# Optimization experiments

Measured on AMD Instinct MI355X. Metric: run time of the kernel, lower is better.

The kernel has to match this reference:

```python
import jax, jax.numpy as jnp
import numpy as np

B, L, KNN = 8, 512, 16
D, H, NL, DLAT = 1024, 16, 2, 64
DH = D // H
DFF = 4 * D
HENC = D // 2          # SwiGLUFFNEncoder hidden = d_model // 2
POS_CLIP = 32
NPOS = 2 * POS_CLIP + 1


def _layernorm(x, g, b, eps=1e-5):
    m = x.mean(-1, keepdims=True)
    v = ((x - m) ** 2).mean(-1, keepdims=True)
    return (x - m) / jnp.sqrt(v + eps) * g + b


def setup_inputs() -> dict:
    key = jax.random.key(0)
    ks = jax.random.split(key, 16)

    def g(i, shape, scale=0.02):
        return jax.random.normal(ks[i], shape, dtype=jnp.float32) * scale

    return {
        "coords": jax.random.normal(ks[0], (B, L, 3, 3), dtype=jnp.float32) * 3.0,
        "eps": jax.random.normal(ks[1], (B, L, DLAT), dtype=jnp.float32),
        "emb": g(2, (NPOS, D)),
        "ln1_g": jnp.ones((NL, D)), "ln1_b": jnp.zeros((NL, D)),
        "Wqkv": g(3, (NL, D, 3 * D)), "bqkv": jnp.zeros((NL, 3 * D)),
        "dist_scale": g(4, (NL, H), 1.0),
        "Wo": g(5, (NL, D, D)), "bo": jnp.zeros((NL, D)),
        "ln2_g": jnp.ones((NL, D)), "ln2_b": jnp.zeros((NL, D)),
        "Wf1": g(6, (NL, D, 2 * DFF)), "bf1": jnp.zeros((NL, 2 * DFF)),
        "Wf2": g(7, (NL, DFF, D)), "bf2": jnp.zeros((NL, D)),
        "lnf_g": jnp.ones((D,)), "lnf_b": jnp.zeros((D,)),
        "We1": g(8, (D, 2 * HENC)), "be1": jnp.zeros((2 * HENC,)),
        "We2": g(9, (HENC, 2 * DLAT)), "be2": jnp.zeros((2 * DLAT,)),
        "attention_mask": jnp.ones((B, L), dtype=bool),
        "sequence_id": jnp.zeros((B, L), dtype=jnp.int32),
    }


def reference(coords, eps, emb, ln1_g, ln1_b, Wqkv, bqkv, dist_scale, Wo, bo,
              ln2_g, ln2_b, Wf1, bf1, Wf2, bf2, lnf_g, lnf_b, We1, be1, We2, be2,
              attention_mask, sequence_id):
    # --- frames: only CA translations feed the geometric attention bias ---
    t = coords[..., 1, :]                       # CA atoms, [B,L,3]

    # --- KNN graph build (no_grad in torch -> stop_gradient) ---
    ca = jax.lax.stop_gradient(t)
    d2 = ((ca[:, :, None, :] - ca[:, None, :, :]) ** 2).sum(-1)   # [B,L,L]
    same_seq = sequence_id[:, :, None] == sequence_id[:, None, :]
    valid = attention_mask[:, None, :] & same_seq
    d2 = jnp.where(valid, d2, jnp.inf)
    _, edges = jax.lax.top_k(-d2, KNN)          # [B,L,KNN]; self is index 0

    def gather(x):  # node_gather: x [B,L,...] -> [B,L,KNN,...]
        return jax.vmap(lambda xb, ib: xb[ib])(x, edges)

    tg = gather(t).reshape(B * L, KNN, 3)                 # neighbor translations
    maskg = gather(attention_mask).reshape(B * L, KNN)

    # --- relative positional embedding (residue_index=None -> knn edges) ---
    res_idxs = edges.reshape(B * L, KNN)
    diff = res_idxs - res_idxs[:, :1]
    z = emb[jnp.clip(diff, -POS_CLIP, POS_CLIP) + POS_CLIP]   # [N,E,D]

    # --- local geometric transformer over the 16-neighbor window ---
    dist = jnp.sqrt(((tg[:, :, None, :] - tg[:, None, :, :]) ** 2).sum(-1) + 1e-8)  # [N,E,E]
    for l in range(NL):
        h = _layernorm(z, ln1_g[l], ln1_b[l])
        qkv = h @ Wqkv[l] + bqkv[l]
        q, k, v = [a.reshape(B * L, KNN, H, DH) for a in jnp.split(qkv, 3, axis=-1)]
        scores = jnp.einsum('nehd,nfhd->nhef', q, k) / np.sqrt(DH).astype(np.float32)
        scores = scores - jax.nn.softplus(dist_scale[l])[None, :, None, None] * dist[:, None]
        scores = jnp.where(maskg[:, None, None, :], scores, -1e9)
        a = jax.nn.softmax(scores, axis=-1)
        o = jnp.einsum('nhef,nfhd->nehd', a, v).reshape(B * L, KNN, D)
        z = z + o @ Wo[l] + bo[l]
        h2 = _layernorm(z, ln2_g[l], ln2_b[l])
        a1, b1 = jnp.split(h2 @ Wf1[l] + bf1[l], 2, axis=-1)
        z = z + (jax.nn.silu(a1) * b1) @ Wf2[l] + bf2[l]

    # --- extract central node, norm, SwiGLU encoder head, reparameterize ---
    zc = z.reshape(B, L, KNN, D)[:, :, 0, :]
    zc = _layernorm(zc, lnf_g, lnf_b)
    zc = jnp.where(attention_mask[..., None], zc, 0.0)
    u1, v1 = jnp.split(zc @ We1 + be1, 2, axis=-1)
    hh = jax.nn.silu(u1) * v1
    mu, logvar = jnp.split(hh @ We2 + be2, 2, axis=-1)
    logvar = jnp.minimum(logvar, 5.0)
    zs = mu + eps * jnp.exp(0.5 * logvar)
    return zs, mu, logvar
```

## Files before the change

### kernel.cpp

```cpp
#include <hip/hip_runtime.h>
#include <hip/hip_bf16.h>
#include <math.h>

#define LLEN 512
#define KNNK 16
#define DIM 1024
#define NHEAD 16
#define NLAYER 2
#define DFFN 4096
#define POSCLIP 32
#define NQ 4096
#define NTOK 65536
#define HSPLIT 4

typedef __attribute__((ext_vector_type(8))) short short8v;
typedef __attribute__((ext_vector_type(4))) float f32x4;
typedef unsigned short ushort_t;

__device__ __forceinline__ float b2f(ushort_t u) {
  union { unsigned u; float f; } x; x.u = ((unsigned)u) << 16; return x.f;
}

__device__ __forceinline__ void xcd_map(int bid, int Mtiles, int Ntiles, int XN,
                                        int& mt, int& nt) {
  int nt_per = Ntiles / XN;
  int mt_per = (Mtiles * XN) >> 3;
  int xcd = bid & 7, i = bid >> 3;
  int xn = xcd % XN, xm = xcd / XN;
  int ntl = i % nt_per, mtl = i / nt_per;
  mt = xm * mt_per + mtl;
  nt = xn * nt_per + ntl;
}

#define GLD16(gp, lp)                                                          \
  __builtin_amdgcn_global_load_lds(                                            \
      (const __attribute__((address_space(1))) void*)(gp),                     \
      (__attribute__((address_space(3))) void*)(lp), 16, 0, 0)

__global__ __launch_bounds__(64) void knn_kernel(const float* __restrict__ coords,
                                                 int* __restrict__ edges) {
  int n = blockIdx.x;
  int b = n / LLEN, i = n % LLEN;
  int lane = threadIdx.x;
  const float* cb = coords + (size_t)b * LLEN * 9;
  float xi = cb[i * 9 + 3], yi = cb[i * 9 + 4], zi = cb[i * 9 + 5];
  float d[8];
#pragma unroll
  for (int r = 0; r < 8; ++r) {
    int j = r * 64 + lane;
    float dx = xi - cb[j * 9 + 3];
    float dy = yi - cb[j * 9 + 4];
    float dz = zi - cb[j * 9 + 5];
    d[r] = dx * dx + dy * dy + dz * dz;
  }
  for (int s = 0; s < KNNK; ++s) {
    float bv = INFINITY; int bi = 1 << 30;
#pragma unroll
    for (int r = 0; r < 8; ++r) {
      int j = r * 64 + lane;
      if (d[r] < bv || (d[r] == bv && j < bi)) { bv = d[r]; bi = j; }
    }
#pragma unroll
    for (int off = 32; off > 0; off >>= 1) {
      float ov = __shfl_xor(bv, off);
      int   oi = __shfl_xor(bi, off);
      if (ov < bv || (ov == bv && oi < bi)) { bv = ov; bi = oi; }
    }
    if (lane == 0) edges[n * KNNK + s] = bi;
    if ((bi & 63) == lane) d[bi >> 6] = INFINITY;
  }
}

__global__ __launch_bounds__(256) void dist_kernel(const float* __restrict__ coords,
                                                   const int* __restrict__ edges,
                                                   float* __restrict__ dist) {
  int n = blockIdx.x; int b = n / LLEN;
  __shared__ float tx[16], ty[16], tz[16];
  int t = threadIdx.x;
  const float* cb = coords + (size_t)b * LLEN * 9;
  if (t < 16) {
    int j = edges[n * KNNK + t];
    tx[t] = cb[j * 9 + 3]; ty[t] = cb[j * 9 + 4]; tz[t] = cb[j * 9 + 5];
  }
  __syncthreads();
  int e = t >> 4, f = t & 15;
  float dx = tx[e] - tx[f], dy = ty[e] - ty[f], dz = tz[e] - tz[f];
  dist[(size_t)n * 256 + t] = sqrtf(dx * dx + dy * dy + dz * dz + 1e-8f);
}

__global__ __launch_bounds__(256) void zinit_kernel(const int* __restrict__ edges,
                                                    const float* __restrict__ emb,
                                                    float* __restrict__ zbuf, int tok0) {
  int tl = blockIdx.x;
  int tok = tok0 + tl;
  int n = tok >> 4;
  int diff = edges[tok] - edges[n << 4];
  int idx = min(max(diff, -POSCLIP), POSCLIP) + POSCLIP;
  ((float4*)(zbuf + (size_t)tl * DIM))[threadIdx.x] =
      ((const float4*)(emb + (size_t)idx * DIM))[threadIdx.x];
}

__global__ __launch_bounds__(256) void ln_kernel(const float* __restrict__ X, int stride,
                                                 const float* __restrict__ g,
                                                 const float* __restrict__ bta,
                                                 __hip_bfloat16* __restrict__ Y) {
  int row = blockIdx.x; int t = threadIdx.x;
  const float4* xr = (const float4*)(X + (size_t)row * stride);
  float4 v = xr[t];
  float s = v.x + v.y + v.z + v.w;
  __shared__ float red[8];
  for (int off = 32; off; off >>= 1) s += __shfl_down(s, off);
  int wid = t >> 6;
  if ((t & 63) == 0) red[wid] = s;
  __syncthreads();
  if (t == 0) red[4] = (red[0] + red[1] + red[2] + red[3]) * (1.0f / DIM);
  __syncthreads();
  float mean = red[4];
  float d0 = v.x - mean, d1 = v.y - mean, d2 = v.z - mean, d3 = v.w - mean;
  float s2 = d0 * d0 + d1 * d1 + d2 * d2 + d3 * d3;
  for (int off = 32; off; off >>= 1) s2 += __shfl_down(s2, off);
  if ((t & 63) == 0) red[wid] = s2;
  __syncthreads();
  if (t == 0) red[5] = rsqrtf((red[0] + red[1] + red[2] + red[3]) * (1.0f / DIM) + 1e-5f);
  __syncthreads();
  float rstd = red[5];
  float4 gv = ((const float4*)g)[t], bv = ((const float4*)bta)[t];
  size_t o = (size_t)row * DIM + t * 4;
  Y[o + 0] = __float2bfloat16(d0 * rstd * gv.x + bv.x);
  Y[o + 1] = __float2bfloat16(d1 * rstd * gv.y + bv.y);
  Y[o + 2] = __float2bfloat16(d2 * rstd * gv.z + bv.z);
  Y[o + 3] = __float2bfloat16(d3 * rstd * gv.w + bv.w);
}

__global__ __launch_bounds__(256) void wconv_kernel(const float* __restrict__ W,
                                                    __hip_bfloat16* __restrict__ Wt,
                                                    int K, int N) {
  __shared__ float tile[32][33];
  int n0 = blockIdx.x * 32, k0 = blockIdx.y * 32;
  int c = threadIdx.x & 31, r = threadIdx.x >> 5;
#pragma unroll
  for (int i = 0; i < 4; ++i)
    tile[r + i * 8][c] = W[(size_t)(k0 + r + i * 8) * N + n0 + c];
  __syncthreads();
#pragma unroll
  for (int i = 0; i < 4; ++i)
    Wt[(size_t)(n0 + r + i * 8) * K + k0 + c] = __float2bfloat16(tile[c][r + i * 8]);
}


template <int MODE>
__global__ __launch_bounds__(256, 3) void gemmT128_kernel(
    const ushort_t* __restrict__ A,
    const ushort_t* __restrict__ Wt,
    const float* __restrict__ bias,
    void* __restrict__ Cout,
    int K, int Mtiles, int Cstride, int Ntiles, int XN) {
  __shared__ ushort_t Alds[3][4096];
  __shared__ ushort_t Blds[3][4096];
  int t = threadIdx.x;
  int w = t >> 6, lane = t & 63;
  int wr = w >> 1, wc = w & 1;
  int fr = lane & 15, kg = lane >> 4;

  int mt, nt;
  xcd_map(blockIdx.x, Mtiles, Ntiles, XN, mt, nt);
  size_t m0 = (size_t)mt * 128, n0 = (size_t)nt * 128;

  int stg_r = w * 16 + (lane >> 2);
  int stg_c = (((lane & 3) ^ ((lane >> 3) & 3)) << 3);
  const ushort_t* gAl = A + (m0 + stg_r) * (size_t)K + stg_c;
  const ushort_t* gBl = Wt + (n0 + stg_r) * (size_t)K + stg_c;
  int lds_w = w * 512;

#define SAt(slot, kcol, j) GLD16(gAl + (size_t)(j) * 64 * K + (kcol), Alds[slot] + (j) * 2048 + lds_w)
#define SBt(slot, kcol, j) GLD16(gBl + (size_t)(j) * 64 * K + (kcol), Blds[slot] + (j) * 2048 + lds_w)

  f32x4 acc[4][4];
#pragma unroll
  for (int i = 0; i < 4; ++i)
#pragma unroll
    for (int j = 0; j < 4; ++j) acc[i][j] = (f32x4){0.f, 0.f, 0.f, 0.f};

  int usw = ((kg ^ ((fr >> 1) & 3)) << 3);

  SAt(0, 0, 0); SAt(0, 0, 1); SBt(0, 0, 0); SBt(0, 0, 1);
  SAt(1, 32, 0); SAt(1, 32, 1); SBt(1, 32, 0); SBt(1, 32, 1);
  asm volatile("s_waitcnt vmcnt(4)" ::: "memory");
  __builtin_amdgcn_s_barrier();

  short8v af[4], bf[4];
  int NT = K >> 5;
  int sl = 0, st = 2;
  for (int ti = 0; ti < NT; ++ti) {
    int kS = (ti + 2) << 5;
    int stg = (ti + 2) < NT;
    const ushort_t* sA = Alds[sl];
    const ushort_t* sB = Blds[sl];
#pragma unroll
    for (int mi = 0; mi < 4; ++mi)
      af[mi] = *(const short8v*)(sA + (wr * 64 + mi * 16 + fr) * 32 + usw);
#pragma unroll
    for (int ni = 0; ni < 4; ++ni)
      bf[ni] = *(const short8v*)(sB + (wc * 64 + ni * 16 + fr) * 32 + usw);
    if (stg) { SAt(st, kS, 0); SAt(st, kS, 1); SBt(st, kS, 0); SBt(st, kS, 1); }
    asm volatile("s_waitcnt lgkmcnt(0)" ::: "memory");
    __builtin_amdgcn_sched_barrier(0);
    __builtin_amdgcn_s_setprio(1);
#pragma unroll
    for (int mi = 0; mi < 4; ++mi)
#pragma unroll
      for (int ni = 0; ni < 4; ++ni)
        acc[mi][ni] = __builtin_amdgcn_mfma_f32_16x16x32_bf16(af[mi], bf[ni], acc[mi][ni], 0, 0, 0);
    __builtin_amdgcn_s_setprio(0);
    if (stg) { asm volatile("s_waitcnt vmcnt(4)" ::: "memory"); }
    else if (ti + 1 < NT) { asm volatile("s_waitcnt vmcnt(0)" ::: "memory"); }
    __builtin_amdgcn_s_barrier();
    sl = (sl == 2) ? 0 : sl + 1;
    st = (st == 2) ? 0 : st + 1;
  }
#undef SAt
#undef SBt

  int er = wr * 64 + (lane >> 4) * 4;
  int ec = wc * 64 + fr;
#pragma unroll
  for (int mi = 0; mi < 4; ++mi) {
#pragma unroll
    for (int ni = 0; ni < 4; ++ni) {
      int col = (int)n0 + ec + ni * 16;
      float bs = bias[col];
#pragma unroll
      for (int j = 0; j < 4; ++j) {
        size_t row = m0 + er + mi * 16 + j;
        size_t cidx = row * (size_t)Cstride + col;
        float x = acc[mi][ni][j] + bs;
        if constexpr (MODE == 0) {
          ((__hip_bfloat16*)Cout)[cidx] = __float2bfloat16(x);
        } else {
          ((float*)Cout)[cidx] += x;
        }
      }
    }
  }
}

__global__ __launch_bounds__(256, 2) void gemmGW_kernel(
    const ushort_t* __restrict__ A,
    const ushort_t* __restrict__ Wt,
    const float* __restrict__ bias,
    __hip_bfloat16* __restrict__ Cout,
    int K, int Mtiles, int Cstride, int NhRows, int Ntiles, int XN) {
  __shared__ ushort_t Alds[3][4096];
  __shared__ ushort_t B1lds[3][4096];
  __shared__ ushort_t B2lds[3][4096];
  int t = threadIdx.x;
  int w = t >> 6, lane = t & 63;
  int wr = w >> 1, wc = w & 1;
  int fr = lane & 15, kg = lane >> 4;

  int mt, nt;
  xcd_map(blockIdx.x, Mtiles, Ntiles, XN, mt, nt);
  size_t m0 = (size_t)mt * 128, n0 = (size_t)nt * 128;

  int stg_r = w * 16 + (lane >> 2);
  int stg_c = (((lane & 3) ^ ((lane >> 3) & 3)) << 3);
  const ushort_t* gAl = A + (m0 + stg_r) * (size_t)K + stg_c;
  const ushort_t* gB1 = Wt + (n0 + stg_r) * (size_t)K + stg_c;
  const ushort_t* gB2 = Wt + ((size_t)NhRows + n0 + stg_r) * (size_t)K + stg_c;
  int lds_w = w * 512;

#define SAg(slot, kcol, j) GLD16(gAl + (size_t)(j) * 64 * K + (kcol), Alds[slot] + (j) * 2048 + lds_w)
#define SB1g(slot, kcol, j) GLD16(gB1 + (size_t)(j) * 64 * K + (kcol), B1lds[slot] + (j) * 2048 + lds_w)
#define SB2g(slot, kcol, j) GLD16(gB2 + (size_t)(j) * 64 * K + (kcol), B2lds[slot] + (j) * 2048 + lds_w)

  f32x4 acc1[4][4], acc2[4][4];
#pragma unroll
  for (int i = 0; i < 4; ++i)
#pragma unroll
    for (int j = 0; j < 4; ++j) {
      acc1[i][j] = (f32x4){0.f, 0.f, 0.f, 0.f};
      acc2[i][j] = (f32x4){0.f, 0.f, 0.f, 0.f};
    }

  int usw = ((kg ^ ((fr >> 1) & 3)) << 3);

  SAg(0, 0, 0); SAg(0, 0, 1); SB1g(0, 0, 0); SB1g(0, 0, 1); SB2g(0, 0, 0); SB2g(0, 0, 1);
  SAg(1, 32, 0); SAg(1, 32, 1); SB1g(1, 32, 0); SB1g(1, 32, 1); SB2g(1, 32, 0); SB2g(1, 32, 1);
  asm volatile("s_waitcnt vmcnt(6)" ::: "memory");
  __builtin_amdgcn_s_barrier();

  short8v af[4], bf1[4], bf2[4];
  int NT = K >> 5;
  int sl = 0, st = 2;
  for (int ti = 0; ti < NT; ++ti) {
    int kS = (ti + 2) << 5;
    int stg = (ti + 2) < NT;
    const ushort_t* sA = Alds[sl];
    const ushort_t* sB1 = B1lds[sl];
    const ushort_t* sB2 = B2lds[sl];
#pragma unroll
    for (int mi = 0; mi < 4; ++mi)
      af[mi] = *(const short8v*)(sA + (wr * 64 + mi * 16 + fr) * 32 + usw);
#pragma unroll
    for (int ni = 0; ni < 4; ++ni) {
      bf1[ni] = *(const short8v*)(sB1 + (wc * 64 + ni * 16 + fr) * 32 + usw);
      bf2[ni] = *(const short8v*)(sB2 + (wc * 64 + ni * 16 + fr) * 32 + usw);
    }
    if (stg) {
      SAg(st, kS, 0); SAg(st, kS, 1);
      SB1g(st, kS, 0); SB1g(st, kS, 1);
      SB2g(st, kS, 0); SB2g(st, kS, 1);
    }
    asm volatile("s_waitcnt lgkmcnt(0)" ::: "memory");
    __builtin_amdgcn_sched_barrier(0);
    __builtin_amdgcn_s_setprio(1);
#pragma unroll
    for (int mi = 0; mi < 4; ++mi)
#pragma unroll
      for (int ni = 0; ni < 4; ++ni) {
        acc1[mi][ni] = __builtin_amdgcn_mfma_f32_16x16x32_bf16(af[mi], bf1[ni], acc1[mi][ni], 0, 0, 0);
        acc2[mi][ni] = __builtin_amdgcn_mfma_f32_16x16x32_bf16(af[mi], bf2[ni], acc2[mi][ni], 0, 0, 0);
      }
    __builtin_amdgcn_s_setprio(0);
    if (stg) { asm volatile("s_waitcnt vmcnt(6)" ::: "memory"); }
    else if (ti + 1 < NT) { asm volatile("s_waitcnt vmcnt(0)" ::: "memory"); }
    __builtin_amdgcn_s_barrier();
    sl = (sl == 2) ? 0 : sl + 1;
    st = (st == 2) ? 0 : st + 1;
  }
#undef SAg
#undef SB1g
#undef SB2g

  int er = wr * 64 + (lane >> 4) * 4;
  int ec = wc * 64 + fr;
#pragma unroll
  for (int mi = 0; mi < 4; ++mi) {
#pragma unroll
    for (int ni = 0; ni < 4; ++ni) {
      int col = (int)n0 + ec + ni * 16;
      float b1v = bias[col];
      float b2v = bias[NhRows + col];
#pragma unroll
      for (int j = 0; j < 4; ++j) {
        size_t row = m0 + er + mi * 16 + j;
        float x1 = acc1[mi][ni][j] + b1v;
        float x2 = acc2[mi][ni][j] + b2v;
        float sg = x1 / (1.f + expf(-x1));
        Cout[row * (size_t)Cstride + col] = __float2bfloat16(sg * x2);
      }
    }
  }
}

template <int MODE>
__global__ __launch_bounds__(256) void mgemm_kernel(
    const __hip_bfloat16* __restrict__ A,
    const __hip_bfloat16* __restrict__ Wt,
    const float* __restrict__ bias,
    void* __restrict__ Cout,
    int K, int Nh, int Cstride) {
  __shared__ ushort_t As[4 * 128 * 8];
  __shared__ ushort_t Bs[4 * 128 * 8];
  __shared__ ushort_t Bs2[(MODE == 2) ? 4 * 128 * 8 : 8];
  int t = threadIdx.x;
  int w = t >> 6, lane = t & 63;
  int wr = w >> 1, wc = w & 1;
  size_t m0 = (size_t)blockIdx.y * 128;
  size_t n0 = (size_t)blockIdx.x * 128;
  int cell0 = w * 64 + lane;
  int cell1 = 256 + w * 64 + lane;
  int kg0 = cell0 >> 7, rw0 = cell0 & 127;
  int kg1 = cell1 >> 7, rw1 = cell1 & 127;
  const ushort_t* gA = (const ushort_t*)A;
  const ushort_t* gB = (const ushort_t*)Wt;
  const ushort_t* gB2 = (const ushort_t*)(Wt + (size_t)Nh * K);
  size_t a0 = (m0 + rw0) * (size_t)K + kg0 * 8;
  size_t a1 = (m0 + rw1) * (size_t)K + kg1 * 8;
  size_t b0 = (n0 + rw0) * (size_t)K + kg0 * 8;
  size_t b1 = (n0 + rw1) * (size_t)K + kg1 * 8;
  int ldso0 = w * 1024;
  int ldso1 = 4096 + w * 1024;
  f32x4 acc[4][4];
  f32x4 acc2[4][4];
#pragma unroll
  for (int i = 0; i < 4; ++i)
#pragma unroll
    for (int j = 0; j < 4; ++j) {
      acc[i][j] = (f32x4){0.f, 0.f, 0.f, 0.f};
      acc2[i][j] = (f32x4){0.f, 0.f, 0.f, 0.f};
    }
  int fr = lane & 15, kg = lane >> 4;
  int abase = (kg * 128 + wr * 64 + fr) * 16;
  int bbase = (kg * 128 + wc * 64 + fr) * 16;
  for (int k0 = 0; k0 < K; k0 += 32) {
    __syncthreads();
    GLD16(gA + a0 + k0, (char*)As + ldso0);
    GLD16(gA + a1 + k0, (char*)As + ldso1);
    GLD16(gB + b0 + k0, (char*)Bs + ldso0);
    GLD16(gB + b1 + k0, (char*)Bs + ldso1);
    if constexpr (MODE == 2) {
      GLD16(gB2 + b0 + k0, (char*)Bs2 + ldso0);
      GLD16(gB2 + b1 + k0, (char*)Bs2 + ldso1);
    }
    __syncthreads();
    short8v a[4], b[4];
#pragma unroll
    for (int mi = 0; mi < 4; ++mi)
      a[mi] = *(const short8v*)((const char*)As + abase + mi * 256);
#pragma unroll
    for (int ni = 0; ni < 4; ++ni)
      b[ni] = *(const short8v*)((const char*)Bs + bbase + ni * 256);
#pragma unroll
    for (int mi = 0; mi < 4; ++mi)
#pragma unroll
      for (int ni = 0; ni < 4; ++ni)
        acc[mi][ni] = __builtin_amdgcn_mfma_f32_16x16x32_bf16(a[mi], b[ni], acc[mi][ni], 0, 0, 0);
    if constexpr (MODE == 2) {
#pragma unroll
      for (int ni = 0; ni < 4; ++ni)
        b[ni] = *(const short8v*)((const char*)Bs2 + bbase + ni * 256);
#pragma unroll
      for (int mi = 0; mi < 4; ++mi)
#pragma unroll
        for (int ni = 0; ni < 4; ++ni)
          acc2[mi][ni] = __builtin_amdgcn_mfma_f32_16x16x32_bf16(a[mi], b[ni], acc2[mi][ni], 0, 0, 0);
    }
  }
  int er = wr * 64 + (lane >> 4) * 4;
  int ec = wc * 64 + fr;
#pragma unroll
  for (int mi = 0; mi < 4; ++mi) {
#pragma unroll
    for (int ni = 0; ni < 4; ++ni) {
      int col = (int)n0 + ec + ni * 16;
      float bs1 = bias[col];
#pragma unroll
      for (int j = 0; j < 4; ++j) {
        size_t row = m0 + er + mi * 16 + j;
        size_t cidx = row * (size_t)Cstride + col;
        float x = acc[mi][ni][j] + bs1;
        if constexpr (MODE == 3) {
          ((float*)Cout)[cidx] = x;
        } else {
          float x2 = acc2[mi][ni][j] + bias[Nh + col];
          float sig = 1.f / (1.f + expf(-x));
          ((__hip_bfloat16*)Cout)[cidx] = __float2bfloat16(x * sig * x2);
        }
      }
    }
  }
}

__global__ __launch_bounds__(256) void attn_kernel(const __hip_bfloat16* __restrict__ qkv,
                                                   const float* __restrict__ dist,
                                                   const float* __restrict__ ds_l,
                                                   __hip_bfloat16* __restrict__ o) {
  int nq = blockIdx.x >> 2;
  int h0 = (blockIdx.x & 3) * (NHEAD / HSPLIT);
  int t = threadIdx.x;
  __shared__ float qs[16][65], ks[16][65], vs[16][65];
  __shared__ float sc[16][17], dl[16][17];
  __shared__ float sps_s[NHEAD];
  dl[t >> 4][t & 15] = dist[(size_t)nq * 256 + t];
  if (t < NHEAD) sps_s[t] = log1pf(expf(ds_l[t]));
  size_t base = (size_t)nq * 16 * 3072;
  int e = t >> 4, c4 = (t & 15) * 4;
  const ushort_t* qp = (const ushort_t*)qkv;
  for (int h = h0; h < h0 + NHEAD / HSPLIT; ++h) {
    const ushort_t* p = qp + base + (size_t)e * 3072 + h * 64 + c4;
    ushort4 qv = *(const ushort4*)p;
    ushort4 kv = *(const ushort4*)(p + 1024);
    ushort4 vv = *(const ushort4*)(p + 2048);
    qs[e][c4] = b2f(qv.x); qs[e][c4 + 1] = b2f(qv.y); qs[e][c4 + 2] = b2f(qv.z); qs[e][c4 + 3] = b2f(qv.w);
    ks[e][c4] = b2f(kv.x); ks[e][c4 + 1] = b2f(kv.y); ks[e][c4 + 2] = b2f(kv.z); ks[e][c4 + 3] = b2f(kv.w);
    vs[e][c4] = b2f(vv.x); vs[e][c4 + 1] = b2f(vv.y); vs[e][c4 + 2] = b2f(vv.z); vs[e][c4 + 3] = b2f(vv.w);
    __syncthreads();
    int ee = t >> 4, ff = t & 15;
    float s = 0.f;
#pragma unroll
    for (int d = 0; d < 64; ++d) s = fmaf(qs[ee][d], ks[ff][d], s);
    sc[ee][ff] = s * 0.125f - sps_s[h] * dl[ee][ff];
    __syncthreads();
    if (t < 16) {
      float m = -1e30f;
      for (int f = 0; f < 16; ++f) m = fmaxf(m, sc[t][f]);
      float sum = 0.f;
      for (int f = 0; f < 16; ++f) { float pe = expf(sc[t][f] - m); sc[t][f] = pe; sum += pe; }
      float inv = 1.f / sum;
      for (int f = 0; f < 16; ++f) sc[t][f] *= inv;
    }
    __syncthreads();
#pragma unroll
    for (int r = 0; r < 4; ++r) {
      int idx = t + 256 * r;
      int oe = idx >> 6, od = idx & 63;
      float acc = 0.f;
#pragma unroll
      for (int f = 0; f < 16; ++f) acc = fmaf(sc[oe][f], vs[f][od], acc);
      o[(size_t)(nq * 16 + oe) * 1024 + h * 64 + od] = __float2bfloat16(acc);
    }
    __syncthreads();
  }
}

__global__ __launch_bounds__(256) void attn2_kernel(const __hip_bfloat16* __restrict__ qkv,
                                                    const float* __restrict__ dist,
                                                    const float* __restrict__ ds_l,
                                                    __hip_bfloat16* __restrict__ o) {
  int nq = blockIdx.x;
  int t = threadIdx.x;
  __shared__ ushort_t ks[16 * 1032];
  __shared__ ushort_t vs[16 * 1032];
  __shared__ float qsf[1024];
  __shared__ float sc[16][17];
  __shared__ float pm[16], pi[16], sps_s[16], dl[16];
  const ushort_t* qp = (const ushort_t*)qkv;
  size_t base = (size_t)nq * 16 * 3072;
#pragma unroll
  for (int i = 0; i < 8; ++i) {
    int flat8 = (i * 256 + t) * 8;
    int e = flat8 >> 10, cc = flat8 & 1023;
    *(short8v*)(ks + e * 1032 + cc) = *(const short8v*)(qp + base + (size_t)e * 3072 + 1024 + cc);
    *(short8v*)(vs + e * 1032 + cc) = *(const short8v*)(qp + base + (size_t)e * 3072 + 2048 + cc);
  }
  {
    ushort4 qv = *(const ushort4*)(qp + base + t * 4);
    qsf[t * 4 + 0] = b2f(qv.x); qsf[t * 4 + 1] = b2f(qv.y);
    qsf[t * 4 + 2] = b2f(qv.z); qsf[t * 4 + 3] = b2f(qv.w);
  }
  if (t < 16) {
    sps_s[t] = log1pf(expf(ds_l[t]));
    dl[t] = dist[(size_t)nq * 256 + t];
  }
  __syncthreads();
  int h = t >> 4, f = t & 15;
  float s = 0.f;
#pragma unroll
  for (int dc = 0; dc < 8; ++dc) {
    short8v k8 = *(const short8v*)(ks + f * 1032 + h * 64 + dc * 8);
#pragma unroll
    for (int j = 0; j < 8; ++j)
      s = fmaf(qsf[h * 64 + dc * 8 + j], b2f((ushort_t)k8[j]), s);
  }
  sc[h][f] = s * 0.125f - sps_s[h] * dl[f];
  __syncthreads();
  if (t < 16) {
    float m = -1e30f;
    for (int ff = 0; ff < 16; ++ff) m = fmaxf(m, sc[t][ff]);
    float sum = 0.f;
    for (int ff = 0; ff < 16; ++ff) sum += expf(sc[t][ff] - m);
    pm[t] = m; pi[t] = 1.f / sum;
  }
  __syncthreads();
  float p = expf(sc[h][f] - pm[h]) * pi[h];
  __syncthreads();
  sc[h][f] = p;
  __syncthreads();
#pragma unroll
  for (int r = 0; r < 4; ++r) {
    int idx = t + 256 * r;
    int oh = idx >> 6, od = idx & 63;
    float acc = 0.f;
#pragma unroll
    for (int f2 = 0; f2 < 16; ++f2)
      acc = fmaf(sc[oh][f2], b2f(vs[f2 * 1032 + oh * 64 + od]), acc);
    o[(size_t)nq * 1024 + idx] = __float2bfloat16(acc);
  }
}

__global__ __launch_bounds__(256) void z0copy_kernel(const float* __restrict__ z,
                                                     float* __restrict__ z0) {
  ((float4*)(z0 + (size_t)blockIdx.x * 1024))[threadIdx.x] =
      ((const float4*)(z + (size_t)blockIdx.x * 16384))[threadIdx.x];
}

__global__ __launch_bounds__(64) void final_kernel(const float* __restrict__ tmp,
                                                   const float* __restrict__ eps,
                                                   float* __restrict__ out) {
  int r = blockIdx.x; int j = threadIdx.x;
  float mu = tmp[r * 128 + j];
  float lv = fminf(tmp[r * 128 + 64 + j], 5.0f);
  float zs = mu + eps[r * 64 + j] * expf(0.5f * lv);
  out[r * 64 + j] = zs;
  out[262144 + r * 64 + j] = mu;
  out[524288 + r * 64 + j] = lv;
}

extern "C" void kernel_launch(void* const* d_in, const int* in_sizes, int n_in,
                              void* d_out, int out_size, void* d_ws, size_t ws_size,
                              hipStream_t stream) {
  (void)in_sizes; (void)n_in; (void)out_size;
  const float* coords = (const float*)d_in[0];
  const float* eps    = (const float*)d_in[1];
  const float* emb    = (const float*)d_in[2];
  const float* ln1_g  = (const float*)d_in[3];
  const float* ln1_b  = (const float*)d_in[4];
  const float* Wqkv   = (const float*)d_in[5];
  const float* bqkv   = (const float*)d_in[6];
  const float* dist_scale = (const float*)d_in[7];
  const float* Wo     = (const float*)d_in[8];
  const float* bo     = (const float*)d_in[9];
  const float* ln2_g  = (const float*)d_in[10];
  const float* ln2_b  = (const float*)d_in[11];
  const float* Wf1    = (const float*)d_in[12];
  const float* bf1    = (const float*)d_in[13];
  const float* Wf2    = (const float*)d_in[14];
  const float* bf2    = (const float*)d_in[15];
  const float* lnf_g  = (const float*)d_in[16];
  const float* lnf_b  = (const float*)d_in[17];
  const float* We1    = (const float*)d_in[18];
  const float* be1    = (const float*)d_in[19];
  const float* We2    = (const float*)d_in[20];
  const float* be2    = (const float*)d_in[21];

  char* ws = (char*)d_ws;
  int*   edges = (int*)ws;
  float* dist  = (float*)(ws + (4ull << 20));
  __hip_bfloat16* hfinal = (__hip_bfloat16*)(ws + (8ull << 20));
  __hip_bfloat16* gated  = (__hip_bfloat16*)(ws + (16ull << 20));
  float* tmp   = (float*)(ws + (20ull << 20));
  __hip_bfloat16* o_all  = (__hip_bfloat16*)(ws + (22ull << 20));
  float* z0_all = (float*)(ws + (30ull << 20));
  __hip_bfloat16* wbase = (__hip_bfloat16*)(ws + (46ull << 20));
  size_t woff = 0;
  __hip_bfloat16* wqkvT = wbase + woff; woff += 2ull * 3072 * 1024;
  __hip_bfloat16* woT   = wbase + woff; woff += 2ull * 1024 * 1024;
  __hip_bfloat16* wf1T  = wbase + woff; woff += 2ull * 8192 * 1024;
  __hip_bfloat16* wf2T  = wbase + woff; woff += 2ull * 1024 * 4096;
  __hip_bfloat16* we1T  = wbase + woff; woff += 1024ull * 1024;
  __hip_bfloat16* we2T  = wbase + woff; woff += 128ull * 512;

  const size_t FIXED = 116ull << 20;
  int CQ = 4096;
  while (CQ > 256 && FIXED + (size_t)CQ * 16 * 14336ull > ws_size) CQ >>= 1;
  if (FIXED + (size_t)CQ * 16 * 14336ull > ws_size) return;
  size_t CT = (size_t)CQ * KNNK;
  char* creg = ws + FIXED;
  float* zbuf = (float*)creg;
  __hip_bfloat16* hbuf = (__hip_bfloat16*)(creg + CT * 4096);
  __hip_bfloat16* sh8  = (__hip_bfloat16*)(creg + CT * 6144);
  __hip_bfloat16* h2        = hbuf;
  __hip_bfloat16* gated_all = sh8;

  knn_kernel<<<NQ, 64, 0, stream>>>(coords, edges);
  dist_kernel<<<NQ, 256, 0, stream>>>(coords, edges, dist);
  for (int l = 0; l < NLAYER; ++l) {
    wconv_kernel<<<dim3(96, 32), 256, 0, stream>>>(Wqkv + (size_t)l * 1024 * 3072,
                                                   wqkvT + (size_t)l * 3072 * 1024, 1024, 3072);
    wconv_kernel<<<dim3(32, 32), 256, 0, stream>>>(Wo + (size_t)l * 1024 * 1024,
                                                   woT + (size_t)l * 1024 * 1024, 1024, 1024);
    wconv_kernel<<<dim3(256, 32), 256, 0, stream>>>(Wf1 + (size_t)l * 1024 * 8192,
                                                    wf1T + (size_t)l * 8192 * 1024, 1024, 8192);
    wconv_kernel<<<dim3(32, 128), 256, 0, stream>>>(Wf2 + (size_t)l * 4096 * 1024,
                                                    wf2T + (size_t)l * 1024 * 4096, 4096, 1024);
  }
  wconv_kernel<<<dim3(32, 32), 256, 0, stream>>>(We1, we1T, 1024, 1024);
  wconv_kernel<<<dim3(4, 16), 256, 0, stream>>>(We2, we2T, 512, 128);

  int NCH = NQ / CQ;
  int MT128 = (int)(CT / 128);
  for (int c = 0; c < NCH; ++c) {
    zinit_kernel<<<(int)CT, 256, 0, stream>>>(edges, emb, zbuf, (int)(c * CT));
    ln_kernel<<<(int)CT, 256, 0, stream>>>(zbuf, DIM, ln1_g, ln1_b, hbuf);
    gemmT128_kernel<0><<<MT128 * 24, 256, 0, stream>>>(
        (const ushort_t*)hbuf, (const ushort_t*)wqkvT, bqkv, sh8, 1024, MT128, 3072, 24, 4);
    attn_kernel<<<CQ * HSPLIT, 256, 0, stream>>>(sh8, dist + (size_t)c * CQ * 256,
                                                 dist_scale, hbuf);
    gemmT128_kernel<1><<<MT128 * 8, 256, 0, stream>>>(
        (const ushort_t*)hbuf, (const ushort_t*)woT, bo, zbuf, 1024, MT128, 1024, 8, 2);
    ln_kernel<<<(int)CT, 256, 0, stream>>>(zbuf, DIM, ln2_g, ln2_b, hbuf);
    gemmGW_kernel<<<MT128 * 32, 256, 0, stream>>>(
        (const ushort_t*)hbuf, (const ushort_t*)wf1T, bf1, sh8, 1024, MT128, 4096, 4096, 32, 4);
    gemmT128_kernel<1><<<MT128 * 8, 256, 0, stream>>>(
        (const ushort_t*)sh8, (const ushort_t*)wf2T, bf2, zbuf, 4096, MT128, 1024, 8, 2);
    ln_kernel<<<(int)CT, 256, 0, stream>>>(zbuf, DIM, ln1_g + DIM, ln1_b + DIM, hbuf);
    gemmT128_kernel<0><<<MT128 * 24, 256, 0, stream>>>(
        (const ushort_t*)hbuf, (const ushort_t*)(wqkvT + 3072ull * 1024),
        bqkv + 3072, sh8, 1024, MT128, 3072, 24, 4);
    attn2_kernel<<<CQ, 256, 0, stream>>>(sh8, dist + (size_t)c * CQ * 256,
                                         dist_scale + NHEAD, o_all + (size_t)c * CQ * 1024);
    z0copy_kernel<<<CQ, 256, 0, stream>>>(zbuf, z0_all + (size_t)c * CQ * 1024);
  }

  int MTQ = NQ / 128;
  gemmT128_kernel<1><<<MTQ * 8, 256, 0, stream>>>(
      (const ushort_t*)o_all, (const ushort_t*)(woT + 1024ull * 1024),
      bo + DIM, z0_all, 1024, MTQ, 1024, 8, 2);
  ln_kernel<<<NQ, 256, 0, stream>>>(z0_all, DIM, ln2_g + DIM, ln2_b + DIM, h2);
  gemmGW_kernel<<<MTQ * 32, 256, 0, stream>>>(
      (const ushort_t*)h2, (const ushort_t*)(wf1T + 8192ull * 1024),
      bf1 + 2 * DFFN, gated_all, 1024, MTQ, 4096, 4096, 32, 4);
  gemmT128_kernel<1><<<MTQ * 8, 256, 0, stream>>>(
      (const ushort_t*)gated_all, (const ushort_t*)(wf2T + 1024ull * 4096),
      bf2 + DIM, z0_all, 4096, MTQ, 1024, 8, 2);
  ln_kernel<<<NQ, 256, 0, stream>>>(z0_all, DIM, lnf_g, lnf_b, hfinal);

  mgemm_kernel<2><<<dim3(4, 32), 256, 0, stream>>>(hfinal, we1T, be1, gated, 1024, 512, 512);
  mgemm_kernel<3><<<dim3(1, 32), 256, 0, stream>>>(gated, we2T, be2, tmp, 512, 0, 128);
  final_kernel<<<NQ, 64, 0, stream>>>(tmp, eps, (float*)d_out);
}
```

Baseline: 4.065 ms.

## Precompute layer-0 LN+QKV over 65 position embeddings and gather per edge

Result: faster. 3.727 ms (-8.3%).

```diff
diff --git a/kernel.cpp b/kernel.cpp
--- a/kernel.cpp
+++ b/kernel.cpp
@@ -145,6 +145,31 @@
 #pragma unroll
   for (int i = 0; i < 4; ++i)
     Wt[(size_t)(n0 + r + i * 8) * K + k0 + c] = __float2bfloat16(tile[c][r + i * 8]);
+}
+
+__global__ __launch_bounds__(256) void qkv65_kernel(const __hip_bfloat16* __restrict__ h65,
+                                                    const __hip_bfloat16* __restrict__ wqkvT,
+                                                    const float* __restrict__ bqkv,
+                                                    __hip_bfloat16* __restrict__ out) {
+  int r = blockIdx.x;
+  int t = threadIdx.x;
+  __shared__ float a[1024];
+  {
+    ushort4 v = *(const ushort4*)((const ushort_t*)h65 + (size_t)r * 1024 + t * 4);
+    a[t * 4 + 0] = b2f(v.x); a[t * 4 + 1] = b2f(v.y);
+    a[t * 4 + 2] = b2f(v.z); a[t * 4 + 3] = b2f(v.w);
+  }
+  __syncthreads();
+  for (int c = t; c < 3072; c += 256) {
+    const ushort_t* wrow = (const ushort_t*)wqkvT + (size_t)c * 1024;
+    float s = 0.f;
+    for (int k = 0; k < 1024; k += 8) {
+      short8v w8 = *(const short8v*)(wrow + k);
+#pragma unroll
+      for (int j = 0; j < 8; ++j) s = fmaf(a[k + j], b2f((ushort_t)w8[j]), s);
+    }
+    out[(size_t)r * 3072 + c] = __float2bfloat16(s + bqkv[c]);
+  }
 }
 
 
@@ -452,23 +477,30 @@
   }
 }
 
-__global__ __launch_bounds__(256) void attn_kernel(const __hip_bfloat16* __restrict__ qkv,
-                                                   const float* __restrict__ dist,
-                                                   const float* __restrict__ ds_l,
-                                                   __hip_bfloat16* __restrict__ o) {
+__global__ __launch_bounds__(256) void attn_g_kernel(const __hip_bfloat16* __restrict__ qkv65,
+                                                     const int* __restrict__ edges,
+                                                     const float* __restrict__ dist,
+                                                     const float* __restrict__ ds_l,
+                                                     __hip_bfloat16* __restrict__ o) {
   int nq = blockIdx.x >> 2;
   int h0 = (blockIdx.x & 3) * (NHEAD / HSPLIT);
   int t = threadIdx.x;
   __shared__ float qs[16][65], ks[16][65], vs[16][65];
   __shared__ float sc[16][17], dl[16][17];
   __shared__ float sps_s[NHEAD];
+  __shared__ int map_s[16];
   dl[t >> 4][t & 15] = dist[(size_t)nq * 256 + t];
   if (t < NHEAD) sps_s[t] = log1pf(expf(ds_l[t]));
-  size_t base = (size_t)nq * 16 * 3072;
+  if (t < 16) {
+    int diff = edges[nq * 16 + t] - edges[nq * 16];
+    map_s[t] = min(max(diff, -POSCLIP), POSCLIP) + POSCLIP;
+  }
+  __syncthreads();
   int e = t >> 4, c4 = (t & 15) * 4;
-  const ushort_t* qp = (const ushort_t*)qkv;
+  const ushort_t* qp = (const ushort_t*)qkv65;
+  size_t ebase = (size_t)map_s[e] * 3072;
   for (int h = h0; h < h0 + NHEAD / HSPLIT; ++h) {
-    const ushort_t* p = qp + base + (size_t)e * 3072 + h * 64 + c4;
+    const ushort_t* p = qp + ebase + h * 64 + c4;
     ushort4 qv = *(const ushort4*)p;
     ushort4 kv = *(const ushort4*)(p + 1024);
     ushort4 vv = *(const ushort4*)(p + 2048);
@@ -630,6 +662,8 @@
   __hip_bfloat16* wf2T  = wbase + woff; woff += 2ull * 1024 * 4096;
   __hip_bfloat16* we1T  = wbase + woff; woff += 1024ull * 1024;
   __hip_bfloat16* we2T  = wbase + woff; woff += 128ull * 512;
+  __hip_bfloat16* h65   = wbase + woff; woff += 65ull * 1024;
+  __hip_bfloat16* qkv65 = wbase + woff; woff += 65ull * 3072;
 
   const size_t FIXED = 116ull << 20;
   int CQ = 4096;
@@ -658,15 +692,16 @@
   wconv_kernel<<<dim3(32, 32), 256, 0, stream>>>(We1, we1T, 1024, 1024);
   wconv_kernel<<<dim3(4, 16), 256, 0, stream>>>(We2, we2T, 512, 128);
 
+  ln_kernel<<<65, 256, 0, stream>>>(emb, DIM, ln1_g, ln1_b, h65);
+  qkv65_kernel<<<65, 256, 0, stream>>>(h65, wqkvT, bqkv, qkv65);
+
   int NCH = NQ / CQ;
   int MT128 = (int)(CT / 128);
   for (int c = 0; c < NCH; ++c) {
     zinit_kernel<<<(int)CT, 256, 0, stream>>>(edges, emb, zbuf, (int)(c * CT));
-    ln_kernel<<<(int)CT, 256, 0, stream>>>(zbuf, DIM, ln1_g, ln1_b, hbuf);
-    gemmT128_kernel<0><<<MT128 * 24, 256, 0, stream>>>(
-        (const ushort_t*)hbuf, (const ushort_t*)wqkvT, bqkv, sh8, 1024, MT128, 3072, 24, 4);
-    attn_kernel<<<CQ * HSPLIT, 256, 0, stream>>>(sh8, dist + (size_t)c * CQ * 256,
-                                                 dist_scale, hbuf);
+    attn_g_kernel<<<CQ * HSPLIT, 256, 0, stream>>>(qkv65, edges + (size_t)c * CQ * 16,
+                                                   dist + (size_t)c * CQ * 256,
+                                                   dist_scale, hbuf);
     gemmT128_kernel<1><<<MT128 * 8, 256, 0, stream>>>(
         (const ushort_t*)hbuf, (const ushort_t*)woT, bo, zbuf, 1024, MT128, 1024, 8, 2);
     ln_kernel<<<(int)CT, 256, 0, stream>>>(zbuf, DIM, ln2_g, ln2_b, hbuf);
```
